# Kernel tuning notes

Hardware: AMD Instinct MI355X
Metric: run time of the kernel (lower is better)

The kernel has to match this reference:

```python
import jax, jax.numpy as jnp
import numpy as np

N_NODES = 100000
N_EDGES = 1000000
IN_FEATS = 128
HID_FEATS = 128
OUT_FEATS = 128
N_CLASSES = 16
NEG_SLOPE = 0.01
BN_EPS = 1e-5


def _linear_params(key, d_in, d_out):
    k1, k2 = jax.random.split(key)
    s = 1.0 / np.sqrt(d_in)
    w = jax.random.uniform(k1, (d_in, d_out), jnp.float32, -s, s)
    b = jax.random.uniform(k2, (d_out,), jnp.float32, -s, s)
    return w, b


def setup_inputs() -> dict:
    key = jax.random.key(0)
    ks = jax.random.split(key, 16)
    node_feat = jax.random.normal(ks[0], (N_NODES, IN_FEATS), jnp.float32)
    src = jax.random.randint(ks[1], (N_EDGES,), 0, N_NODES, jnp.int32)
    dst = jax.random.randint(ks[2], (N_EDGES,), 0, N_NODES, jnp.int32)
    dims = [(IN_FEATS, HID_FEATS), (HID_FEATS, HID_FEATS), (HID_FEATS, OUT_FEATS)]
    inp = {"node_feat": node_feat, "src": src, "dst": dst}
    for i, (din, dout) in enumerate(dims):
        wp, bp = _linear_params(ks[3 + 4 * i], din, din)      # fc_pool: d_in -> d_in
        ws, _ = _linear_params(ks[4 + 4 * i], din, dout)       # fc_self (no bias)
        wn, _ = _linear_params(ks[5 + 4 * i], din, dout)       # fc_neigh (no bias)
        _, b = _linear_params(ks[6 + 4 * i], din, dout)        # shared output bias
        inp[f"wp{i}"] = wp; inp[f"bp{i}"] = bp
        inp[f"ws{i}"] = ws; inp[f"wn{i}"] = wn; inp[f"b{i}"] = b
    inp["bn_gamma"] = jnp.ones((HID_FEATS,), jnp.float32)
    inp["bn_beta"] = jnp.zeros((HID_FEATS,), jnp.float32)
    wc, bc = _linear_params(ks[15], OUT_FEATS, N_CLASSES)
    inp["wc"] = wc; inp["bc"] = bc
    return inp


def _sage_pool(h, src, dst, deg_mask, wp, bp, ws, wn, b):
    # fc_pool + relu on source nodes, gather per edge, segment-max to dst
    hp = jax.nn.relu(h @ wp + bp)                 # [N, d_in]
    msg = hp[src]                                 # [E, d_in]
    agg = jax.ops.segment_max(msg, dst, num_segments=N_NODES)  # [N, d_in]
    agg = jnp.where(deg_mask, agg, 0.0)           # zero for isolated nodes
    return h @ ws + agg @ wn + b


def _batchnorm(x, gamma, beta):
    mu = jnp.mean(x, axis=0)
    var = jnp.var(x, axis=0)
    return (x - mu) * jax.lax.rsqrt(var + BN_EPS) * gamma + beta


def reference(node_feat, src, dst,
              wp0, bp0, ws0, wn0, b0,
              wp1, bp1, ws1, wn1, b1,
              wp2, bp2, ws2, wn2, b2,
              bn_gamma, bn_beta, wc, bc):
    deg = jnp.zeros((N_NODES,), jnp.float32).at[dst].add(1.0)
    deg_mask = (deg > 0)[:, None]
    h = jax.nn.leaky_relu(_sage_pool(node_feat, src, dst, deg_mask, wp0, bp0, ws0, wn0, b0), NEG_SLOPE)
    h = jax.nn.leaky_relu(_batchnorm(_sage_pool(h, src, dst, deg_mask, wp1, bp1, ws1, wn1, b1), bn_gamma, bn_beta), NEG_SLOPE)
    h = _sage_pool(h, src, dst, deg_mask, wp2, bp2, ws2, wn2, b2)
    return h @ wc + bc
```

## Files before the change

kernel.cpp:

```cpp
#include <hip/hip_runtime.h>


#define N_NODES 100000
#define N_EDGES 1000000
#define F 128
#define NEG_SLOPE 0.01f
#define BN_EPS 1e-5f
#define NODES_PER_XCD 12500

typedef __attribute__((ext_vector_type(8))) short bf16x8;
typedef __attribute__((ext_vector_type(4))) float f32x4;

typedef __attribute__((address_space(3))) unsigned int as3_uint;
typedef __attribute__((address_space(1))) const unsigned int as1_cuint;

__device__ __forceinline__ void gload16(const void* g, void* l) {
    __builtin_amdgcn_global_load_lds((as1_cuint*)g, (as3_uint*)l, 16, 0, 0);
}

__device__ __forceinline__ unsigned short f2bf(float f) {
    unsigned int u = __float_as_uint(f);
    u += 0x7fff + ((u >> 16) & 1);
    return (unsigned short)(u >> 16);
}
__device__ __forceinline__ float bf2f(unsigned short h) {
    return __uint_as_float(((unsigned int)h) << 16);
}

__global__ __launch_bounds__(256) void zero_kernel(float4* __restrict__ p, long n4) {
    long i = (long)blockIdx.x * 256 + threadIdx.x;
    if (i < n4) p[i] = make_float4(0.f, 0.f, 0.f, 0.f);
}

__global__ __launch_bounds__(256) void f32_to_bf16_kernel(
    const float4* __restrict__ in, uint2* __restrict__ out, long n4)
{
    long i = (long)blockIdx.x * 256 + threadIdx.x;
    if (i >= n4) return;
    float4 v = in[i];
    uint2 o;
    o.x = (unsigned)f2bf(v.x) | ((unsigned)f2bf(v.y) << 16);
    o.y = (unsigned)f2bf(v.z) | ((unsigned)f2bf(v.w) << 16);
    out[i] = o;
}

__global__ __launch_bounds__(256) void pack_weights3(
    const float* __restrict__ wp, const float* __restrict__ wss,
    const float* __restrict__ wn, short* __restrict__ wp_p, short* __restrict__ wsn_p)
{
    const int i = blockIdx.x * 256 + threadIdx.x;
    if (i >= 3 * 16384) return;
    const int mat = i >> 14;
    const int idx = i & 16383;
    const int k = idx >> 7, n = idx & 127;
    const float* srcm = mat == 0 ? wp : (mat == 1 ? wss : wn);
    const int slot = ((k >> 3) * 128 + n) * 8 + (k & 7);
    if (mat == 0) wp_p[slot] = (short)f2bf(srcm[idx]);
    else wsn_p[(mat == 2 ? 16 * 128 * 8 : 0) + slot] = (short)f2bf(srcm[idx]);
}

template<int NKS>
__global__ __launch_bounds__(256) void gemm_mfma(
    const short* __restrict__ A1, const short* __restrict__ A2,
    const short* __restrict__ Bp, const float* __restrict__ bias,
    unsigned short* __restrict__ Cout, int n_rows, int act)
{
    constexpr int S = NKS / 2;
    __shared__ short tile[2 * 8192];

    const int tid = threadIdx.x;
    const int wave = tid >> 6;
    const int lane = tid & 63;
    const int m = lane & 15, q = lane >> 4;
    const int r0 = blockIdx.x * 128;
    const int rw = (wave >> 1) * 64;
    const int r0q = r0 + rw;
    const int c0 = (wave & 1) * 64;
    const int gchunk = (tid & 7) ^ ((tid >> 3) & 7);

    f32x4 acc[4][4];
#pragma unroll
    for (int i = 0; i < 4; ++i)
#pragma unroll
        for (int j = 0; j < 4; ++j)
#pragma unroll
            for (int r = 0; r < 4; ++r) acc[i][j][r] = 0.f;

    auto stage = [&](int s, int buf) {
        const short* Ap = (NKS == 8 && s >= 2) ? A2 : A1;
        const int kbase = (s & 1) * 64;
#pragma unroll
        for (int p = 0; p < 4; ++p) {
            int row = r0 + (tid >> 3) + 32 * p;
            row = min(row, n_rows - 1);
            gload16(Ap + (size_t)row * F + kbase + gchunk * 8,
                    &tile[buf * 8192 + p * 2048 + tid * 8]);
        }
    };

    stage(0, 0);
    __syncthreads();

    for (int s = 0; s < S; ++s) {
        if (s + 1 < S) stage(s + 1, (s + 1) & 1);
        const short* tb = &tile[(s & 1) * 8192];
#pragma unroll
        for (int ks2 = 0; ks2 < 2; ++ks2) {
            const int ks32 = s * 2 + ks2;
            bf16x8 b[4], a[4];
#pragma unroll
            for (int ni = 0; ni < 4; ++ni)
                b[ni] = *(const bf16x8*)(Bp + ((size_t)(ks32 * 4 + q) * F + c0 + ni * 16 + m) * 8);
#pragma unroll
            for (int mi = 0; mi < 4; ++mi)
                a[mi] = *(const bf16x8*)(tb + (rw + mi * 16 + m) * 64 + (((ks2 * 4 + q) ^ (m & 7)) << 3));
#pragma unroll
            for (int mi = 0; mi < 4; ++mi)
#pragma unroll
                for (int ni = 0; ni < 4; ++ni)
                    acc[mi][ni] = __builtin_amdgcn_mfma_f32_16x16x32_bf16(a[mi], b[ni], acc[mi][ni], 0, 0, 0);
        }
        __syncthreads();
    }

    float bv[4];
#pragma unroll
    for (int ni = 0; ni < 4; ++ni) bv[ni] = bias[c0 + ni * 16 + m];

    short* ep = &tile[wave * 1280];
    const int colc_lo = m >> 3, cin = m & 7;
#pragma unroll
    for (int mi = 0; mi < 4; ++mi) {
#pragma unroll
        for (int ni = 0; ni < 4; ++ni) {
            const int colc = 2 * ni + colc_lo;
#pragma unroll
            for (int rg = 0; rg < 4; ++rg) {
                const int row16 = q * 4 + rg;
                float v = acc[mi][ni][rg] + bv[ni];
                if (act == 1) v = v > 0.f ? v : 0.f;
                else if (act == 2) v = v > 0.f ? v : v * NEG_SLOPE;
                ep[row16 * 80 + ((colc ^ (row16 & 7)) << 3) + cin] = (short)f2bf(v);
            }
        }
        __syncthreads();
#pragma unroll
        for (int p = 0; p < 2; ++p) {
            const int lrow = (lane >> 3) + 8 * p;
            bf16x8 vv = *(const bf16x8*)&ep[lrow * 80 + (((lane & 7) ^ (lrow & 7)) << 3)];
            const int grow = r0q + mi * 16 + lrow;
            if (grow < n_rows)
                *(bf16x8*)(Cout + (size_t)grow * F + c0 + ((lane & 7) << 3)) = vv;
        }
        __syncthreads();
    }
}

__global__ __launch_bounds__(256) void hist_kernel(const int* __restrict__ dst, int* __restrict__ deg) {
    const int e = blockIdx.x * 256 + threadIdx.x;
    if (e < N_EDGES) atomicAdd(&deg[__builtin_nontemporal_load(&dst[e])], 1);
}

__global__ __launch_bounds__(256) void scan1_kernel(const int* __restrict__ deg, int* __restrict__ bsum) {
    __shared__ int sh[256];
    const int t = threadIdx.x;
    const int base = blockIdx.x * 1024 + t * 4;
    int s = 0;
#pragma unroll
    for (int j = 0; j < 4; ++j) s += (base + j < N_NODES) ? deg[base + j] : 0;
    sh[t] = s; __syncthreads();
    for (int off = 128; off; off >>= 1) {
        if (t < off) sh[t] += sh[t + off];
        __syncthreads();
    }
    if (t == 0) bsum[blockIdx.x] = sh[0];
}

__global__ __launch_bounds__(128) void scan2_kernel(int* __restrict__ bsum, int nb, int* __restrict__ row_start) {
    __shared__ int sh[128];
    const int t = threadIdx.x;
    sh[t] = (t < nb) ? bsum[t] : 0;
    __syncthreads();
    for (int off = 1; off < 128; off <<= 1) {
        int x = (t >= off) ? sh[t - off] : 0;
        __syncthreads();
        if (t >= off) sh[t] += x;
        __syncthreads();
    }
    if (t < nb) bsum[t] = t ? sh[t - 1] : 0;
    if (t == 0) row_start[N_NODES] = N_EDGES;
}

__global__ __launch_bounds__(256) void scan3_kernel(
    const int* __restrict__ deg, const int* __restrict__ boff,
    int* __restrict__ row_start, int* __restrict__ cursor)
{
    __shared__ int sh[256];
    const int t = threadIdx.x;
    const int base = blockIdx.x * 1024 + t * 4;
    int v[4]; int s = 0;
#pragma unroll
    for (int j = 0; j < 4; ++j) { v[j] = (base + j < N_NODES) ? deg[base + j] : 0; s += v[j]; }
    sh[t] = s; __syncthreads();
    for (int off = 1; off < 256; off <<= 1) {
        int x = (t >= off) ? sh[t - off] : 0;
        __syncthreads();
        if (t >= off) sh[t] += x;
        __syncthreads();
    }
    int excl = (t ? sh[t - 1] : 0) + boff[blockIdx.x];
#pragma unroll
    for (int j = 0; j < 4; ++j) {
        if (base + j < N_NODES) { row_start[base + j] = excl; cursor[base + j] = excl; }
        excl += v[j];
    }
}

#define CHUNK_E2 1954
__global__ __launch_bounds__(256) void scatter_xcd_kernel(
    const int* __restrict__ src, const int* __restrict__ dst,
    int* __restrict__ cursor, int* __restrict__ esrc)
{
    const int range = blockIdx.x & 7;
    const int chunk = blockIdx.x >> 3;
    const int lo = range * NODES_PER_XCD;
    const int e0 = chunk * CHUNK_E2;
    const int e1 = min(e0 + CHUNK_E2, N_EDGES);
    for (int e = e0 + threadIdx.x; e < e1; e += 256) {
        const int d = dst[e];
        if ((unsigned)(d - lo) < NODES_PER_XCD) {
            const int pos = atomicAdd(&cursor[d], 1);
            esrc[pos] = src[e];
        }
    }
}

__global__ __launch_bounds__(256) void aggregate_max_bf16(
    const unsigned int* __restrict__ hp, const int* __restrict__ row_start,
    const int* __restrict__ esrc, unsigned int* __restrict__ agg)
{
    const int node = blockIdx.x * 4 + (threadIdx.x >> 6);
    if (node >= N_NODES) return;
    const int lane = threadIdx.x & 63;
    const int beg = row_start[node], end = row_start[node + 1];
    unsigned int m0 = 0, m1 = 0;
    int i = beg;
    for (; i + 7 < end; i += 8) {
        unsigned int v[8];
#pragma unroll
        for (int j = 0; j < 8; ++j) v[j] = hp[(size_t)esrc[i + j] * 64 + lane];
#pragma unroll
        for (int j = 0; j < 8; ++j) {
            m0 = max(m0, v[j] & 0xffffu);
            m1 = max(m1, v[j] >> 16);
        }
    }
    if (i + 3 < end) {
        unsigned int v[4];
#pragma unroll
        for (int j = 0; j < 4; ++j) v[j] = hp[(size_t)esrc[i + j] * 64 + lane];
#pragma unroll
        for (int j = 0; j < 4; ++j) {
            m0 = max(m0, v[j] & 0xffffu);
            m1 = max(m1, v[j] >> 16);
        }
        i += 4;
    }
    if (i + 1 < end) {
        const unsigned int a = hp[(size_t)esrc[i] * 64 + lane];
        const unsigned int b = hp[(size_t)esrc[i + 1] * 64 + lane];
        m0 = max(m0, max(a & 0xffffu, b & 0xffffu));
        m1 = max(m1, max(a >> 16, b >> 16));
        i += 2;
    }
    if (i < end) {
        const unsigned int a = hp[(size_t)esrc[i] * 64 + lane];
        m0 = max(m0, a & 0xffffu);
        m1 = max(m1, a >> 16);
    }
    agg[(size_t)node * 64 + lane] = m0 | (m1 << 16);
}

#define BN_ROWS_PER_BLOCK 196
__global__ __launch_bounds__(256) void bn_stats_kernel(
    const unsigned short* __restrict__ x, float* __restrict__ stats, int n)
{
    const int tid = threadIdx.x;
    const int wave = tid >> 6, lane = tid & 63;
    const int rgrp = lane >> 4;
    const int c16 = lane & 15;
    const int rbase = blockIdx.x * BN_ROWS_PER_BLOCK;
    const int rend = min(rbase + BN_ROWS_PER_BLOCK, n);

    float s[8], ss[8];
#pragma unroll
    for (int j = 0; j < 8; ++j) { s[j] = 0.f; ss[j] = 0.f; }

    for (int r = rbase + wave * 4 + rgrp; r < rend; r += 16) {
        const uint4 v = *(const uint4*)(x + (size_t)r * F + c16 * 8);
        const unsigned int w[4] = {v.x, v.y, v.z, v.w};
#pragma unroll
        for (int u = 0; u < 4; ++u) {
            const float f0 = bf2f((unsigned short)(w[u] & 0xffffu));
            const float f1 = bf2f((unsigned short)(w[u] >> 16));
            s[2*u]   += f0; ss[2*u]   = fmaf(f0, f0, ss[2*u]);
            s[2*u+1] += f1; ss[2*u+1] = fmaf(f1, f1, ss[2*u+1]);
        }
    }
#pragma unroll
    for (int j = 0; j < 8; ++j) {
        s[j]  += __shfl_down(s[j], 32);  s[j]  += __shfl_down(s[j], 16);
        ss[j] += __shfl_down(ss[j], 32); ss[j] += __shfl_down(ss[j], 16);
    }
    __shared__ float sh[4][16][16];
    if (lane < 16) {
#pragma unroll
        for (int j = 0; j < 8; ++j) {
            sh[wave][c16][2*j]     = s[j];
            sh[wave][c16][2*j + 1] = ss[j];
        }
    }
    __syncthreads();
    const float tot = sh[0][tid >> 4][tid & 15] + sh[1][tid >> 4][tid & 15]
                    + sh[2][tid >> 4][tid & 15] + sh[3][tid >> 4][tid & 15];
    const int col = (tid >> 4) * 8 + ((tid >> 1) & 7);
    atomicAdd(&stats[(tid & 1) * 128 + col], tot);
}

__global__ void bn_finalize_kernel(
    const float* __restrict__ stats, const float* __restrict__ gamma,
    const float* __restrict__ beta, float* __restrict__ coef)
{
    const int c = threadIdx.x;
    const float mean = stats[c] * (1.f / N_NODES);
    const float var = stats[128 + c] * (1.f / N_NODES) - mean * mean;
    const float scale = gamma[c] * rsqrtf(var + BN_EPS);
    coef[c] = scale;
    coef[128 + c] = fmaf(-mean, scale, beta[c]);
}

__global__ __launch_bounds__(256) void bn_apply_bf16(
    unsigned int* __restrict__ x, const float* __restrict__ coef, long n2)
{
    __shared__ float sc[128], sf[128];
    if (threadIdx.x < 128) {
        sc[threadIdx.x] = coef[threadIdx.x];
        sf[threadIdx.x] = coef[128 + threadIdx.x];
    }
    __syncthreads();
    const long i = (long)blockIdx.x * 256 + threadIdx.x;
    if (i >= n2) return;
    const unsigned int v = x[i];
    const int c0 = (int)(i & 63) * 2;
    float a = fmaf(bf2f((unsigned short)(v & 0xffffu)), sc[c0], sf[c0]);
    float b = fmaf(bf2f((unsigned short)(v >> 16)), sc[c0 + 1], sf[c0 + 1]);
    a = a > 0.f ? a : a * NEG_SLOPE;
    b = b > 0.f ? b : b * NEG_SLOPE;
    x[i] = (unsigned)f2bf(a) | ((unsigned)f2bf(b) << 16);
}

__global__ __launch_bounds__(256) void classifier_kernel(
    const unsigned short* __restrict__ X, const float* __restrict__ Wc,
    const float* __restrict__ bc, float* __restrict__ out, int n)
{
    __shared__ float Wl[2048];
    __shared__ float Xs[16 * 132];
    const int tid = threadIdx.x;
    for (int i = tid; i < 2048; i += 256) Wl[i] = Wc[i];
    const int r0 = blockIdx.x * 16;
    for (int i = tid; i < 2048; i += 256) {
        const int row = i >> 7, col = i & 127;
        const int gr = r0 + row;
        Xs[row * 132 + col] = (gr < n) ? bf2f(X[(size_t)gr * F + col]) : 0.f;
    }
    __syncthreads();
    const int rl = tid >> 4, c = tid & 15;
    const int r = r0 + rl;
    if (r >= n) return;
    float s = bc[c];
    const float* xr = &Xs[rl * 132];
#pragma unroll
    for (int k = 0; k < 128; ++k) s = fmaf(xr[k], Wl[k * 16 + c], s);
    out[(size_t)r * 16 + c] = s;
}

extern "C" void kernel_launch(void* const* d_in, const int* in_sizes, int n_in,
                              void* d_out, int out_size, void* d_ws, size_t ws_size,
                              hipStream_t stream) {
    const float* node_feat = (const float*)d_in[0];
    const int* src = (const int*)d_in[1];
    const int* dst = (const int*)d_in[2];
    const float* wp[3] = {(const float*)d_in[3],  (const float*)d_in[8],  (const float*)d_in[13]};
    const float* bp[3] = {(const float*)d_in[4],  (const float*)d_in[9],  (const float*)d_in[14]};
    const float* wsm[3] = {(const float*)d_in[5], (const float*)d_in[10], (const float*)d_in[15]};
    const float* wn[3] = {(const float*)d_in[6],  (const float*)d_in[11], (const float*)d_in[16]};
    const float* bb[3] = {(const float*)d_in[7],  (const float*)d_in[12], (const float*)d_in[17]};
    const float* gamma = (const float*)d_in[18];
    const float* beta  = (const float*)d_in[19];
    const float* wc    = (const float*)d_in[20];
    const float* bc    = (const float*)d_in[21];

    const size_t SZ = (size_t)N_NODES * F;
    short* sbase = (short*)d_ws;
    short* B0  = sbase;
    short* B1  = sbase + SZ;
    short* B2  = sbase + 2 * SZ;
    short* Xbf = sbase + 3 * SZ;
    short* wp_p  = sbase + 4 * SZ;
    short* wsn_p = wp_p + 3 * 16384;
    float* fbase = (float*)(wsn_p + 3 * 32768);
    float* stats = fbase;
    float* coef  = fbase + 256;
    int* ibase = (int*)(fbase + 512);
    int* deg       = ibase;
    int* row_start = ibase + 100000;
    int* cursor    = ibase + 200104;
    int* esrc      = ibase + 300104;
    int* bsum      = ibase + 1300104;

    const int gGemm = (N_NODES + 127) / 128;
    const int gE    = (N_EDGES + 255) / 256;
    const int gScan = (N_NODES + 1023) / 1024;
    const int gAgg  = (N_NODES + 3) / 4;
    const long cvt4 = (long)(SZ / 4);
    const long n2   = (long)(SZ / 2);

    f32_to_bf16_kernel<<<(int)((cvt4 + 255) / 256), 256, 0, stream>>>(
        (const float4*)node_feat, (uint2*)Xbf, cvt4);
    for (int l = 0; l < 3; ++l)
        pack_weights3<<<192, 256, 0, stream>>>(wp[l], wsm[l], wn[l],
                                               wp_p + l * 16384, wsn_p + l * 32768);

    zero_kernel<<<98, 256, 0, stream>>>((float4*)deg, 25000);
    hist_kernel<<<gE, 256, 0, stream>>>(dst, deg);
    scan1_kernel<<<gScan, 256, 0, stream>>>(deg, bsum);
    scan2_kernel<<<1, 128, 0, stream>>>(bsum, gScan, row_start);
    scan3_kernel<<<gScan, 256, 0, stream>>>(deg, bsum, row_start, cursor);
    scatter_xcd_kernel<<<4096, 256, 0, stream>>>(src, dst, cursor, esrc);

    const short* Xl[3]  = {Xbf, B0, B1};
    short* hpb[3]       = {B0, B1, B0};
    short* aggb[3]      = {B1, B2, B2};
    short* Yb[3]        = {B0, B1, B0};
    for (int l = 0; l < 3; ++l) {
        const short* X = Xl[l];
        gemm_mfma<4><<<gGemm, 256, 0, stream>>>(X, (const short*)nullptr,
            wp_p + l * 16384, bp[l], (unsigned short*)hpb[l], N_NODES, 1);
        aggregate_max_bf16<<<gAgg, 256, 0, stream>>>(
            (const unsigned int*)hpb[l], row_start, esrc, (unsigned int*)aggb[l]);
        const int act = (l == 0) ? 2 : 0;
        gemm_mfma<8><<<gGemm, 256, 0, stream>>>(X, aggb[l],
            wsn_p + l * 32768, bb[l], (unsigned short*)Yb[l], N_NODES, act);
        if (l == 1) {
            zero_kernel<<<1, 256, 0, stream>>>((float4*)stats, 64);
            bn_stats_kernel<<<512, 256, 0, stream>>>(
                (const unsigned short*)Yb[l], stats, N_NODES);
            bn_finalize_kernel<<<1, 128, 0, stream>>>(stats, gamma, beta, coef);
            bn_apply_bf16<<<(int)((n2 + 255) / 256), 256, 0, stream>>>(
                (unsigned int*)Yb[l], coef, n2);
        }
    }
    classifier_kernel<<<(N_NODES + 15) / 16, 256, 0, stream>>>(
        (const unsigned short*)B0, wc, bc, (float*)d_out, N_NODES);
}
```

Before: 553.3 us.

## Store pooled features in 16-column slices so each aggregation pass stays cache-resident

The pool GEMM now writes its output as 8 column slices of 16 bf16 features per node, each slice contiguous across all nodes. The neighbor-max aggregation then runs one block group per slice, and the self/neigh GEMM reads the aggregate back in the same sliced layout. Each slice's gathered working set (about 3.2 MB) is meant to fit in the XCD's L2, cutting random-gather traffic to HBM. In exchange the edge list is read 8 times, each gather moves only 32-byte rows, a shuffle reduction is added, and the aggregation launches 8 times as many blocks.

Result: slower. 936.0 us (+69.2%).

```diff
diff --git a/kernel.cpp b/kernel.cpp
--- a/kernel.cpp
+++ b/kernel.cpp
@@ -7,6 +7,7 @@
 #define NEG_SLOPE 0.01f
 #define BN_EPS 1e-5f
 #define NODES_PER_XCD 12500
+#define SLICE_STRIDE ((size_t)N_NODES * 16)
 
 typedef __attribute__((ext_vector_type(8))) short bf16x8;
 typedef __attribute__((ext_vector_type(4))) float f32x4;
@@ -59,7 +60,7 @@
     else wsn_p[(mat == 2 ? 16 * 128 * 8 : 0) + slot] = (short)f2bf(srcm[idx]);
 }
 
-template<int NKS>
+template<int NKS, bool SLICED_OUT, bool SLICED_A2>
 __global__ __launch_bounds__(256) void gemm_mfma(
     const short* __restrict__ A1, const short* __restrict__ A2,
     const short* __restrict__ Bp, const float* __restrict__ bias,
@@ -87,14 +88,23 @@
             for (int r = 0; r < 4; ++r) acc[i][j][r] = 0.f;
 
     auto stage = [&](int s, int buf) {
-        const short* Ap = (NKS == 8 && s >= 2) ? A2 : A1;
         const int kbase = (s & 1) * 64;
 #pragma unroll
         for (int p = 0; p < 4; ++p) {
             int row = r0 + (tid >> 3) + 32 * p;
             row = min(row, n_rows - 1);
-            gload16(Ap + (size_t)row * F + kbase + gchunk * 8,
-                    &tile[buf * 8192 + p * 2048 + tid * 8]);
+            const short* gp;
+            if (NKS == 8 && s >= 2) {
+                if (SLICED_A2) {
+                    const int cg = (s & 1) * 8 + gchunk;
+                    gp = A2 + (size_t)(cg >> 1) * SLICE_STRIDE + (size_t)row * 16 + (cg & 1) * 8;
+                } else {
+                    gp = A2 + (size_t)row * F + kbase + gchunk * 8;
+                }
+            } else {
+                gp = A1 + (size_t)row * F + kbase + gchunk * 8;
+            }
+            gload16(gp, &tile[buf * 8192 + p * 2048 + tid * 8]);
         }
     };
 
@@ -149,8 +159,14 @@
             const int lrow = (lane >> 3) + 8 * p;
             bf16x8 vv = *(const bf16x8*)&ep[lrow * 80 + (((lane & 7) ^ (lrow & 7)) << 3)];
             const int grow = r0q + mi * 16 + lrow;
-            if (grow < n_rows)
-                *(bf16x8*)(Cout + (size_t)grow * F + c0 + ((lane & 7) << 3)) = vv;
+            if (grow < n_rows) {
+                if (SLICED_OUT) {
+                    const int cg = (c0 >> 3) + (lane & 7);
+                    *(bf16x8*)(Cout + (size_t)(cg >> 1) * SLICE_STRIDE + (size_t)grow * 16 + (cg & 1) * 8) = vv;
+                } else {
+                    *(bf16x8*)(Cout + (size_t)grow * F + c0 + ((lane & 7) << 3)) = vv;
+                }
+            }
         }
         __syncthreads();
     }
@@ -235,50 +251,32 @@
     }
 }
 
-__global__ __launch_bounds__(256) void aggregate_max_bf16(
-    const unsigned int* __restrict__ hp, const int* __restrict__ row_start,
-    const int* __restrict__ esrc, unsigned int* __restrict__ agg)
-{
-    const int node = blockIdx.x * 4 + (threadIdx.x >> 6);
+__global__ __launch_bounds__(256) void aggregate_max_sliced(
+    const unsigned short* __restrict__ hpS, const int* __restrict__ row_start,
+    const int* __restrict__ esrc, unsigned short* __restrict__ aggS)
+{
+    const int s = blockIdx.x & 7;
+    const int node = (blockIdx.x >> 3) * 4 + (threadIdx.x >> 6);
     if (node >= N_NODES) return;
     const int lane = threadIdx.x & 63;
+    const int e8 = lane >> 3, cp = lane & 7;
+    const unsigned short* hps = hpS + (size_t)s * SLICE_STRIDE;
     const int beg = row_start[node], end = row_start[node + 1];
     unsigned int m0 = 0, m1 = 0;
-    int i = beg;
-    for (; i + 7 < end; i += 8) {
-        unsigned int v[8];
-#pragma unroll
-        for (int j = 0; j < 8; ++j) v[j] = hp[(size_t)esrc[i + j] * 64 + lane];
-#pragma unroll
-        for (int j = 0; j < 8; ++j) {
-            m0 = max(m0, v[j] & 0xffffu);
-            m1 = max(m1, v[j] >> 16);
-        }
-    }
-    if (i + 3 < end) {
-        unsigned int v[4];
-#pragma unroll
-        for (int j = 0; j < 4; ++j) v[j] = hp[(size_t)esrc[i + j] * 64 + lane];
-#pragma unroll
-        for (int j = 0; j < 4; ++j) {
-            m0 = max(m0, v[j] & 0xffffu);
-            m1 = max(m1, v[j] >> 16);
-        }
-        i += 4;
-    }
-    if (i + 1 < end) {
-        const unsigned int a = hp[(size_t)esrc[i] * 64 + lane];
-        const unsigned int b = hp[(size_t)esrc[i + 1] * 64 + lane];
-        m0 = max(m0, max(a & 0xffffu, b & 0xffffu));
-        m1 = max(m1, max(a >> 16, b >> 16));
-        i += 2;
-    }
-    if (i < end) {
-        const unsigned int a = hp[(size_t)esrc[i] * 64 + lane];
-        m0 = max(m0, a & 0xffffu);
-        m1 = max(m1, a >> 16);
-    }
-    agg[(size_t)node * 64 + lane] = m0 | (m1 << 16);
+    for (int i = beg + e8; i < end; i += 8) {
+        const int sn = esrc[i];
+        const unsigned int v = *(const unsigned int*)(hps + (size_t)sn * 16 + cp * 2);
+        m0 = max(m0, v & 0xffffu);
+        m1 = max(m1, v >> 16);
+    }
+#pragma unroll
+    for (int off = 32; off >= 8; off >>= 1) {
+        m0 = max(m0, (unsigned int)__shfl_down((int)m0, off));
+        m1 = max(m1, (unsigned int)__shfl_down((int)m1, off));
+    }
+    if (lane < 8)
+        *(unsigned int*)(aggS + (size_t)s * SLICE_STRIDE + (size_t)node * 16 + lane * 2)
+            = m0 | (m1 << 16);
 }
 
 #define BN_ROWS_PER_BLOCK 196
@@ -421,7 +419,7 @@
     const int gGemm = (N_NODES + 127) / 128;
     const int gE    = (N_EDGES + 255) / 256;
     const int gScan = (N_NODES + 1023) / 1024;
-    const int gAgg  = (N_NODES + 3) / 4;
+    const int gAgg  = ((N_NODES + 3) / 4) * 8;
     const long cvt4 = (long)(SZ / 4);
     const long n2   = (long)(SZ / 2);
 
@@ -444,12 +442,12 @@
     short* Yb[3]        = {B0, B1, B0};
     for (int l = 0; l < 3; ++l) {
         const short* X = Xl[l];
-        gemm_mfma<4><<<gGemm, 256, 0, stream>>>(X, (const short*)nullptr,
+        gemm_mfma<4, true, false><<<gGemm, 256, 0, stream>>>(X, (const short*)nullptr,
             wp_p + l * 16384, bp[l], (unsigned short*)hpb[l], N_NODES, 1);
-        aggregate_max_bf16<<<gAgg, 256, 0, stream>>>(
-            (const unsigned int*)hpb[l], row_start, esrc, (unsigned int*)aggb[l]);
+        aggregate_max_sliced<<<gAgg, 256, 0, stream>>>(
+            (const unsigned short*)hpb[l], row_start, esrc, (unsigned short*)aggb[l]);
         const int act = (l == 0) ? 2 : 0;
-        gemm_mfma<8><<<gGemm, 256, 0, stream>>>(X, aggb[l],
+        gemm_mfma<8, false, true><<<gGemm, 256, 0, stream>>>(X, aggb[l],
             wsn_p + l * 32768, bb[l], (unsigned short*)Yb[l], N_NODES, act);
         if (l == 1) {
             zero_kernel<<<1, 256, 0, stream>>>((float4*)stats, 64);
```
